# Optimization experiments

Hardware: AMD Instinct MI355X
Metric: run time of the kernel (lower is better)

The kernel has to match this reference:

```python
import jax, jax.numpy as jnp
import numpy as np

EPS = 1e-12  # torch F.normalize clamps the norm at eps


def diff_sign(x):
    # straight-through estimator: forward = sign (-1/+1), backward = identity
    sign = 2.0 * (x >= 0).astype(x.dtype) - 1.0
    return x + jax.lax.stop_gradient(sign - x)


def setup_inputs() -> dict:
    key = jax.random.key(0)
    k0, k1, k2 = jax.random.split(key, 3)
    B, H, W, C = 64, 32, 32, 512
    bits = 16
    x = jax.random.normal(k0, (B, H, W, C), dtype=jnp.float32)
    # torch Linear init: U(-1/sqrt(fan_in), 1/sqrt(fan_in)); exact dist irrelevant for correctness
    s1 = 1.0 / np.sqrt(C)
    Wp = jax.random.uniform(k1, (C, bits), jnp.float32, -s1, s1)
    bp = jnp.zeros((bits,), jnp.float32)
    s2 = 1.0 / np.sqrt(bits)
    Wr = jax.random.uniform(k2, (bits, C), jnp.float32, -s2, s2)
    br = jnp.zeros((C,), jnp.float32)
    return {"x": x, "Wp": Wp, "bp": bp, "Wr": Wr, "br": br}


def reference(x, Wp, bp, Wr, br):
    B, H, W, C = x.shape
    t = x.reshape(B, H * W, C)                      # [B, HW, C]
    z = jnp.einsum('btc,cd->btd', t, Wp) + bp       # [B, HW, bits]
    norm = jnp.sqrt(jnp.sum(z * z, axis=-1, keepdims=True))
    z = z / jnp.maximum(norm, EPS)                  # F.normalize(p=2, dim=-1)
    code = diff_sign(z).reshape(B, H, W, -1)        # [B, H, W, bits]
    recon = jnp.einsum('bhwd,dc->bhwc', code, Wr) + br
    return recon
```

## Files before the change

kernel.cpp:

```cpp
#include <hip/hip_runtime.h>
#include <stdint.h>


#define ROWS   65536
#define TILE   32
#define BLOCKS (ROWS / TILE)
#define TAU    1e-3f

#define BAR()    asm volatile("s_waitcnt lgkmcnt(0)\n\ts_barrier" ::: "memory")
#define WAITV(N) asm volatile("s_waitcnt vmcnt(" #N ")" ::: "memory")
#define WAITL()  asm volatile("s_waitcnt lgkmcnt(0)" ::: "memory")
#define CFENCE() asm volatile("" ::: "memory")

typedef const __attribute__((address_space(1))) void* gas1_t;
typedef __attribute__((address_space(3))) void*       las3_t;
typedef float v2f __attribute__((ext_vector_type(2)));

__global__ __launch_bounds__(256, 2)
void bsq_fused(const float* __restrict__ x,
               const float* __restrict__ Wp,
               const float* __restrict__ bp,
               const float* __restrict__ Wr,
               const float* __restrict__ br,
               float* __restrict__ out)
{
    const int tid = threadIdx.x;
    const int w   = tid >> 6;
    const int l   = tid & 63;
    const int cg  = l >> 4;
    const int dg  = l & 15;

    __shared__ __align__(16) float  xl[4 * 1024];
    __shared__ __align__(16) float  zp[TILE][16][4];
    __shared__ __align__(16) double zb64[4][16];

    v2f wpA[8], wpB[8];
#pragma unroll
    for (int j = 0; j < 8; ++j) {
        const float* wj = Wp + (w * 128 + j * 16 + cg * 4) * 16 + dg;
        wpA[j] = (v2f){ wj[0],  wj[16] };
        wpB[j] = (v2f){ wj[32], wj[48] };
    }
    const float bpf = bp[dg];

    const int row0 = blockIdx.x * TILE;
    const float* xsrc = x + (size_t)row0 * 512 + (size_t)(l >> 5) * 512
                          + w * 128 + (l & 31) * 4;

    auto stage = [&](int s) {
        __builtin_amdgcn_global_load_lds(
            (gas1_t)(xsrc + (size_t)(2 * s) * 512),
            (las3_t)(&xl[(s & 3) * 1024 + w * 256]), 16, 0, 0);
    };

    auto dot_part = [&](int s, int p, v2f& accA, v2f& accB) {
        const float* bx = &xl[(s & 3) * 1024 + w * 256 + p * 128 + cg * 4];
        float4 xr[8];
#pragma unroll
        for (int j = 0; j < 8; ++j) xr[j] = *(const float4*)(bx + j * 16);
        accA = (v2f){0.f, 0.f};  accB = (v2f){0.f, 0.f};
#pragma unroll
        for (int j = 0; j < 8; ++j) {
            accA += (v2f){ xr[j].x, xr[j].y } * wpA[j];
            accB += (v2f){ xr[j].z, xr[j].w } * wpB[j];
        }
    };
    auto fin_part = [&](int r, v2f accA, v2f accB) {
        float a = (accA.x + accA.y) + (accB.x + accB.y);
        a += __shfl_xor(a, 16, 64);
        a += __shfl_xor(a, 32, 64);
        if (l < 16) zp[r][l][w] = a;
    };

#pragma unroll
    for (int s = 0; s < 4; ++s) stage(s);
#pragma unroll 1
    for (int c = 0; c < 8; ++c) {
        WAITV(3);
        v2f aA0, aB0, aA1, aB1;
        dot_part(c, 0, aA0, aB0);
        dot_part(c, 1, aA1, aB1);
        CFENCE();
        WAITL();
        stage(c + 4);
        CFENCE();
        fin_part(2 * c, aA0, aB0);
        fin_part(2 * c + 1, aA1, aB1);
    }
    BAR();

    v2f wrv[16];
    const float2* Wr2 = (const float2*)Wr;
#pragma unroll
    for (int d = 0; d < 16; ++d) {
        const float2 t = Wr2[d * 256 + tid];
        wrv[d] = (v2f){ t.x, t.y };
    }
    const float2 brt = ((const float2*)br)[tid];
    const v2f br2v = (v2f){ brt.x, brt.y };
    WAITV(0);

    uint32_t amb = 0;
    auto recon_row = [&](int r) {
        const float4 q = *(const float4*)&zp[r][dg][0];
        const float  z = (q.x + q.y) + (q.z + q.w) + bpf;
        if (__ballot(fabsf(z) < TAU)) amb |= (1u << r);
        const int m = (int)(__ballot(z >= 0.0f) & 0xFFFFull);
        v2f o = br2v;
#pragma unroll
        for (int d = 0; d < 16; ++d) {
            const float s = ((m >> d) & 1) ? 1.0f : -1.0f;
            o += (v2f){ s, s } * wrv[d];
        }
        ((float2*)out)[(size_t)(row0 + r) * 256 + tid] = make_float2(o.x, o.y);
    };

#pragma unroll 1
    for (int c = 8; c < 12; ++c) {
        v2f aA0, aB0, aA1, aB1;
        dot_part(c, 0, aA0, aB0);
        dot_part(c, 1, aA1, aB1);
        CFENCE();
        WAITL();
        stage(c + 4);
        CFENCE();
        fin_part(2 * c, aA0, aB0);
        fin_part(2 * c + 1, aA1, aB1);
        recon_row(2 * (c - 8));
        recon_row(2 * (c - 8) + 1);
    }
    {
        v2f aA0, aB0, aA1, aB1;
        WAITV(11);
        dot_part(12, 0, aA0, aB0); dot_part(12, 1, aA1, aB1);
        fin_part(24, aA0, aB0); fin_part(25, aA1, aB1);
        recon_row(8);  recon_row(9);
        WAITV(10);
        dot_part(13, 0, aA0, aB0); dot_part(13, 1, aA1, aB1);
        fin_part(26, aA0, aB0); fin_part(27, aA1, aB1);
        recon_row(10); recon_row(11);
        WAITV(9);
        dot_part(14, 0, aA0, aB0); dot_part(14, 1, aA1, aB1);
        fin_part(28, aA0, aB0); fin_part(29, aA1, aB1);
        recon_row(12); recon_row(13);
        WAITV(8);
        dot_part(15, 0, aA0, aB0); dot_part(15, 1, aA1, aB1);
        fin_part(30, aA0, aB0); fin_part(31, aA1, aB1);
        recon_row(14); recon_row(15);
    }
    BAR();

#pragma unroll 2
    for (int r = 16; r < TILE; ++r) recon_row(r);

    const double bpd = (double)bpf;
#pragma unroll 1
    while (amb) {
        const int r = __ffs(amb) - 1;
        amb &= amb - 1;
        const int row = row0 + r;

        const float* xp = x + (size_t)row * 512 + w * 128 + cg * 4;
        double ad = 0.0;
#pragma unroll
        for (int j = 0; j < 8; ++j) {
            const float4 xf = *(const float4*)(xp + j * 16);
#pragma unroll
            for (int e = 0; e < 4; ++e) {
                const float wpe = Wp[(w * 128 + j * 16 + cg * 4 + e) * 16 + dg];
                const float xe  = e == 0 ? xf.x : e == 1 ? xf.y
                               : e == 2 ? xf.z : xf.w;
                ad = fma((double)xe, (double)wpe, ad);
            }
        }
        ad += __shfl_xor(ad, 16, 64);
        ad += __shfl_xor(ad, 32, 64);
        if (l < 16) zb64[w][l] = ad;
        BAR();
        const double zd = (zb64[0][dg] + zb64[1][dg])
                        + (zb64[2][dg] + zb64[3][dg]) + bpd;
        const int m = (int)(__ballot(zd >= 0.0) & 0xFFFFull);
        BAR();

        v2f o = br2v;
#pragma unroll
        for (int d = 0; d < 16; ++d) {
            const float s = ((m >> d) & 1) ? 1.0f : -1.0f;
            o += (v2f){ s, s } * wrv[d];
        }
        ((float2*)out)[(size_t)row * 256 + tid] = make_float2(o.x, o.y);
    }
}

extern "C" void kernel_launch(void* const* d_in, const int* in_sizes, int n_in,
                              void* d_out, int out_size, void* d_ws, size_t ws_size,
                              hipStream_t stream) {
    const float* x  = (const float*)d_in[0];
    const float* Wp = (const float*)d_in[1];
    const float* bp = (const float*)d_in[2];
    const float* Wr = (const float*)d_in[3];
    const float* br = (const float*)d_in[4];
    float* out = (float*)d_out;

    bsq_fused<<<BLOCKS, 256, 0, stream>>>(x, Wp, bp, Wr, br, out);
}
```

Before: 64.66 us.

## Separate projection from reconstruction and widen output stores to float4

Reconstruction rows are no longer interleaved with the projection's staged loads. The kernel now finishes all 32 projection rows first, then reconstructs with each half of the block handling alternate rows and writing float4 instead of float2. Because each wave now sees different rows, the ambiguity bitmask is merged across waves through shared memory. Wider stores and simpler control flow are traded for losing the overlap of output writes with input prefetch, and a full vmcnt wait is added right after the initial staging.

```diff
diff --git a/kernel.cpp b/kernel.cpp
--- a/kernel.cpp
+++ b/kernel.cpp
@@ -30,9 +30,10 @@
     const int cg  = l >> 4;
     const int dg  = l & 15;
 
-    __shared__ __align__(16) float  xl[4 * 1024];
-    __shared__ __align__(16) float  zp[TILE][16][4];
-    __shared__ __align__(16) double zb64[4][16];
+    __shared__ __align__(16) float    xl[4 * 1024];
+    __shared__ __align__(16) float    zp[TILE][16][4];
+    __shared__ __align__(16) double   zb64[4][16];
+    __shared__            uint32_t    ambx[4];
 
     v2f wpA[8], wpB[8];
 #pragma unroll
@@ -74,8 +75,10 @@
 
 #pragma unroll
     for (int s = 0; s < 4; ++s) stage(s);
+    WAITV(0);
+
 #pragma unroll 1
-    for (int c = 0; c < 8; ++c) {
+    for (int c = 0; c < 12; ++c) {
         WAITV(3);
         v2f aA0, aB0, aA1, aB1;
         dot_part(c, 0, aA0, aB0);
@@ -87,78 +90,57 @@
         fin_part(2 * c, aA0, aB0);
         fin_part(2 * c + 1, aA1, aB1);
     }
+    {
+        v2f aA0, aB0, aA1, aB1;
+        WAITV(3); dot_part(12, 0, aA0, aB0); dot_part(12, 1, aA1, aB1);
+        fin_part(24, aA0, aB0); fin_part(25, aA1, aB1);
+        WAITV(2); dot_part(13, 0, aA0, aB0); dot_part(13, 1, aA1, aB1);
+        fin_part(26, aA0, aB0); fin_part(27, aA1, aB1);
+        WAITV(1); dot_part(14, 0, aA0, aB0); dot_part(14, 1, aA1, aB1);
+        fin_part(28, aA0, aB0); fin_part(29, aA1, aB1);
+        WAITV(0); dot_part(15, 0, aA0, aB0); dot_part(15, 1, aA1, aB1);
+        fin_part(30, aA0, aB0); fin_part(31, aA1, aB1);
+    }
     BAR();
 
-    v2f wrv[16];
-    const float2* Wr2 = (const float2*)Wr;
+    const int col = tid & 127;
+    float4 wr4[16];
 #pragma unroll
-    for (int d = 0; d < 16; ++d) {
-        const float2 t = Wr2[d * 256 + tid];
-        wrv[d] = (v2f){ t.x, t.y };
-    }
-    const float2 brt = ((const float2*)br)[tid];
-    const v2f br2v = (v2f){ brt.x, brt.y };
-    WAITV(0);
+    for (int d = 0; d < 16; ++d) wr4[d] = ((const float4*)Wr)[d * 128 + col];
+    const float4 br4 = ((const float4*)br)[col];
+    const int rp_row = tid >> 7;
 
     uint32_t amb = 0;
-    auto recon_row = [&](int r) {
+#pragma unroll 4
+    for (int rp = 0; rp < 16; ++rp) {
+        const int r = 2 * rp + rp_row;
         const float4 q = *(const float4*)&zp[r][dg][0];
         const float  z = (q.x + q.y) + (q.z + q.w) + bpf;
         if (__ballot(fabsf(z) < TAU)) amb |= (1u << r);
         const int m = (int)(__ballot(z >= 0.0f) & 0xFFFFull);
-        v2f o = br2v;
+
+        v2f o01 = { br4.x, br4.y }, o23 = { br4.z, br4.w };
 #pragma unroll
         for (int d = 0; d < 16; ++d) {
             const float s = ((m >> d) & 1) ? 1.0f : -1.0f;
-            o += (v2f){ s, s } * wrv[d];
+            const v2f sv = { s, s };
+            o01 += sv * (v2f){ wr4[d].x, wr4[d].y };
+            o23 += sv * (v2f){ wr4[d].z, wr4[d].w };
         }
-        ((float2*)out)[(size_t)(row0 + r) * 256 + tid] = make_float2(o.x, o.y);
-    };
+        ((float4*)out)[(size_t)(row0 + r) * 128 + col] =
+            make_float4(o01.x, o01.y, o23.x, o23.y);
+    }
 
-#pragma unroll 1
-    for (int c = 8; c < 12; ++c) {
-        v2f aA0, aB0, aA1, aB1;
-        dot_part(c, 0, aA0, aB0);
-        dot_part(c, 1, aA1, aB1);
-        CFENCE();
-        WAITL();
-        stage(c + 4);
-        CFENCE();
-        fin_part(2 * c, aA0, aB0);
-        fin_part(2 * c + 1, aA1, aB1);
-        recon_row(2 * (c - 8));
-        recon_row(2 * (c - 8) + 1);
-    }
-    {
-        v2f aA0, aB0, aA1, aB1;
-        WAITV(11);
-        dot_part(12, 0, aA0, aB0); dot_part(12, 1, aA1, aB1);
-        fin_part(24, aA0, aB0); fin_part(25, aA1, aB1);
-        recon_row(8);  recon_row(9);
-        WAITV(10);
-        dot_part(13, 0, aA0, aB0); dot_part(13, 1, aA1, aB1);
-        fin_part(26, aA0, aB0); fin_part(27, aA1, aB1);
-        recon_row(10); recon_row(11);
-        WAITV(9);
-        dot_part(14, 0, aA0, aB0); dot_part(14, 1, aA1, aB1);
-        fin_part(28, aA0, aB0); fin_part(29, aA1, aB1);
-        recon_row(12); recon_row(13);
-        WAITV(8);
-        dot_part(15, 0, aA0, aB0); dot_part(15, 1, aA1, aB1);
-        fin_part(30, aA0, aB0); fin_part(31, aA1, aB1);
-        recon_row(14); recon_row(15);
-    }
+    if (l == 0) ambx[w] = amb;
     BAR();
-
-#pragma unroll 2
-    for (int r = 16; r < TILE; ++r) recon_row(r);
+    uint32_t amb_all = ambx[0] | ambx[1] | ambx[2] | ambx[3];
 
     const double bpd = (double)bpf;
 #pragma unroll 1
-    while (amb) {
-        const int r = __ffs(amb) - 1;
-        amb &= amb - 1;
-        const int row = row0 + r;
+    while (amb_all) {
+        const int rr = __ffs(amb_all) - 1;
+        amb_all &= amb_all - 1;
+        const int row = row0 + rr;
 
         const float* xp = x + (size_t)row * 512 + w * 128 + cg * 4;
         double ad = 0.0;
@@ -182,13 +164,17 @@
         const int m = (int)(__ballot(zd >= 0.0) & 0xFFFFull);
         BAR();
 
-        v2f o = br2v;
+        v2f o01 = { br4.x, br4.y }, o23 = { br4.z, br4.w };
 #pragma unroll
         for (int d = 0; d < 16; ++d) {
             const float s = ((m >> d) & 1) ? 1.0f : -1.0f;
-            o += (v2f){ s, s } * wrv[d];
+            const v2f sv = { s, s };
+            o01 += sv * (v2f){ wr4[d].x, wr4[d].y };
+            o23 += sv * (v2f){ wr4[d].z, wr4[d].w };
         }
-        ((float2*)out)[(size_t)row * 256 + tid] = make_float2(o.x, o.y);
+        if (rp_row == (rr & 1))
+            ((float4*)out)[(size_t)row * 128 + col] =
+                make_float4(o01.x, o01.y, o23.x, o23.y);
     }
 }
 
```

After: 73.88 us. +14.3%, slower.
